# Performance work log

Hardware: AMD Instinct MI355X
Metric: run time of the kernel (lower is better)

The kernel has to match this reference:

```python
import jax, jax.numpy as jnp
import numpy as np

NUM_NODES = 10000  # fixed by input spec: edge_index values in [0, 10000)


def setup_inputs() -> dict:
    key = jax.random.key(0)
    k1, k2, k3 = jax.random.split(key, 3)
    N, E, D_IN, D_OUT = NUM_NODES, 320000, 256, 256
    x = jax.random.normal(k1, (N, D_IN), dtype=jnp.float32)
    edge_index = jax.random.randint(k2, (2, E), 0, N, dtype=jnp.int64)
    # ensure node N-1 appears so num_nodes == N as in the torch code
    edge_index = edge_index.at[0, 0].set(N - 1)
    # xavier_uniform for [D_IN, D_OUT]
    limit = float(np.sqrt(6.0 / (D_IN + D_OUT)))
    weight = jax.random.uniform(k3, (D_IN, D_OUT), dtype=jnp.float32,
                                minval=-limit, maxval=limit)
    return {"x": x, "edge_index": edge_index, "weight": weight}


def _normalize_adjacency(edge_index, num_nodes):
    src, dst = edge_index[0], edge_index[1]
    ones = jnp.ones(src.shape[0], dtype=jnp.float32)
    # symmetric binarized adjacency: adj[i,j] = adj[j,i] = 1 (set, not add)
    adj = jnp.zeros((num_nodes, num_nodes), dtype=jnp.float32)
    adj = adj.at[src, dst].max(ones)
    adj = adj.at[dst, src].max(ones)
    # one round of self-loops: adj += I
    adj = adj + jnp.eye(num_nodes, dtype=jnp.float32)
    deg = jnp.sum(adj, axis=1)                    # [N]
    dinv = 1.0 / jnp.sqrt(deg)                    # [N]
    # D^-1/2 A D^-1/2 via broadcasting (equivalent to diag mms)
    return adj * dinv[:, None] * dinv[None, :]


def reference(x, edge_index, weight):
    adj = _normalize_adjacency(edge_index, NUM_NODES)  # [N, N]
    h = adj @ x                                        # [N, D_IN]
    return h @ weight                                  # [N, D_OUT]
```

## Files before the change

### kernel.cpp

```cpp
#include <hip/hip_runtime.h>
#include <hip/hip_bf16.h>
#include <stdint.h>

#define N_NODES   10000
#define D_FEAT    256
#define E_EDGES   320000
#define ROW_WORDS 313
#define ROW_STRIDE 320
#define LIST_CAP  1024

#define NB    250
#define RPB   40
#define B_CAP 8192

#define LDSTR 264

typedef __attribute__((ext_vector_type(4))) float float4v;
typedef _Float16 half8  __attribute__((ext_vector_type(8)));
typedef _Float16 half4v __attribute__((ext_vector_type(4)));

__device__ __forceinline__ uint16_t f2bf(float f) {
    union { float f; uint32_t u; } v; v.f = f;
    uint32_t r = v.u + 0x7fffu + ((v.u >> 16) & 1u);
    return (uint16_t)(r >> 16);
}
__device__ __forceinline__ float lo16(uint32_t u) {
    union { uint32_t u; float f; } v; v.u = u << 16; return v.f;
}
__device__ __forceinline__ float hi16(uint32_t u) {
    union { uint32_t u; float f; } v; v.u = u & 0xffff0000u; return v.f;
}


__global__ void __launch_bounds__(1024)
fill_buckets(const int* __restrict__ ei, uint32_t* __restrict__ bucketbuf,
             uint32_t* __restrict__ cursors) {
    __shared__ uint32_t hist[256];
    __shared__ uint32_t lofs[256];
    __shared__ uint32_t base_s[256];
    __shared__ uint32_t stage[2048];
    __shared__ uint16_t sbkt[2048];
    int t = threadIdx.x;
    if (t < 256) hist[t] = 0;
    __syncthreads();
    int e = blockIdx.x * 1024 + t;
    int b0 = -1, b1 = -1; uint32_t ent0 = 0, ent1 = 0, s0 = 0, s1 = 0;
    if (e < E_EDGES) {
        int s = ei[e], d = ei[E_EDGES + e];
        if ((uint32_t)s < N_NODES && (uint32_t)d < N_NODES) {
            b0 = s / RPB; ent0 = ((uint32_t)(s - b0 * RPB) << 14) | (uint32_t)d;
            b1 = d / RPB; ent1 = ((uint32_t)(d - b1 * RPB) << 14) | (uint32_t)s;
            s0 = atomicAdd(&hist[b0], 1u);
            s1 = atomicAdd(&hist[b1], 1u);
        }
    }
    __syncthreads();
    if (t < 256) lofs[t] = hist[t];
    __syncthreads();
    for (int d = 1; d < 256; d <<= 1) {
        uint32_t v = 0;
        if (t < 256 && t >= d) v = lofs[t - d];
        __syncthreads();
        if (t < 256) lofs[t] += v;
        __syncthreads();
    }
    if (t < 256) base_s[t] = hist[t] ? atomicAdd(&cursors[t], hist[t]) : 0u;
    if (b0 >= 0) {
        uint32_t p0 = lofs[b0] - hist[b0] + s0;
        stage[p0] = ent0; sbkt[p0] = (uint16_t)b0;
        uint32_t p1 = lofs[b1] - hist[b1] + s1;
        stage[p1] = ent1; sbkt[p1] = (uint16_t)b1;
    }
    __syncthreads();
    uint32_t total = lofs[255];
    for (uint32_t idx = t; idx < total; idx += 1024) {
        uint32_t b = sbkt[idx];
        uint32_t pos = base_s[b] + (idx - (lofs[b] - hist[b]));
        if (pos < B_CAP) bucketbuf[(size_t)b * B_CAP + pos] = stage[idx];
    }
}

__global__ void __launch_bounds__(1024)
bucket_to_csr(const uint32_t* __restrict__ bucketbuf,
              const uint32_t* __restrict__ cursors,
              uint32_t* __restrict__ gcursor,
              uint32_t* __restrict__ col, uint32_t* __restrict__ row_base,
              uint32_t* __restrict__ row_deg, float* __restrict__ dinv) {
    __shared__ uint32_t bm[RPB * ROW_WORDS];
    __shared__ uint32_t degs[RPB];
    __shared__ uint32_t rowoff[RPB];
    __shared__ uint32_t segbase;
    int b = blockIdx.x, t = threadIdx.x;
    for (int i = t; i < RPB * ROW_WORDS; i += 1024) bm[i] = 0;
    __syncthreads();
    uint32_t cnt = min(cursors[b], (uint32_t)B_CAP);
    const uint32_t* bb = bucketbuf + (size_t)b * B_CAP;
    for (uint32_t i = t; i < cnt; i += 1024) {
        uint32_t ent = bb[i];
        uint32_t lr = ent >> 14, d = ent & 0x3FFFu;
        atomicOr(&bm[lr * ROW_WORDS + (d >> 5)], 1u << (d & 31));
    }
    __syncthreads();
    int wv = t >> 6, lane = t & 63;
    for (int r = wv; r < RPB; r += 16) {
        int pop = 0;
        #pragma unroll
        for (int k = 0; k < 5; k++) {
            int w = lane + 64 * k;
            if (w < ROW_WORDS) pop += __popc(bm[r * ROW_WORDS + w]);
        }
        #pragma unroll
        for (int off = 32; off > 0; off >>= 1) pop += __shfl_xor(pop, off, 64);
        if (lane == 0) degs[r] = (uint32_t)pop;
    }
    __syncthreads();
    if (t == 0) {
        uint32_t run = 0;
        for (int r = 0; r < RPB; r++) {
            rowoff[r] = run;
            run += (degs[r] + 3u) & ~3u;
        }
        segbase = atomicAdd(gcursor, run);
    }
    __syncthreads();
    int row0 = b * RPB;
    for (int r = wv; r < RPB; r += 16) {
        int gi = row0 + r;
        uint32_t base = segbase + rowoff[r];
        if (lane == 0) {
            row_base[gi] = base;
            row_deg[gi]  = degs[r];
            dinv[gi]     = 1.0f / sqrtf((float)(degs[r] + 1u));
        }
        uint32_t wb[5]; int tot = 0;
        #pragma unroll
        for (int k = 0; k < 5; k++) {
            int w = lane + 64 * k;
            uint32_t v = (w < ROW_WORDS) ? bm[r * ROW_WORDS + w] : 0u;
            wb[k] = v; tot += __popc(v);
        }
        int incl = tot;
        #pragma unroll
        for (int off = 1; off < 64; off <<= 1) {
            int v = __shfl_up(incl, off, 64);
            if (lane >= off) incl += v;
        }
        uint32_t p = base + (uint32_t)(incl - tot);
        #pragma unroll
        for (int k = 0; k < 5; k++) {
            uint32_t bits = wb[k];
            uint32_t cbase = (uint32_t)(lane + 64 * k) << 5;
            while (bits) {
                col[p++] = cbase + (uint32_t)__builtin_ctz(bits);
                bits &= bits - 1;
            }
        }
    }
}

__global__ void __launch_bounds__(256)
scale_cast(const float* __restrict__ dinv, const float* __restrict__ x,
           uint16_t* __restrict__ xs) {
    int wv = threadIdx.x >> 6, lane = threadIdx.x & 63;
    int i = blockIdx.x * 4 + wv;
    float di = dinv[i];
    float4v v = *(const float4v*)(x + (size_t)i * D_FEAT + lane * 4);
    uint2 o;
    o.x = (uint32_t)f2bf(di * v[0]) | ((uint32_t)f2bf(di * v[1]) << 16);
    o.y = (uint32_t)f2bf(di * v[2]) | ((uint32_t)f2bf(di * v[3]) << 16);
    *(uint2*)(xs + (size_t)i * D_FEAT + lane * 4) = o;
}

__global__ void __launch_bounds__(256)
wcast(const float* __restrict__ w, _Float16* __restrict__ wt) {
    int k = blockIdx.x, n = threadIdx.x;
    wt[(size_t)n * D_FEAT + k] = (_Float16)w[(size_t)k * D_FEAT + n];
}

__global__ void __launch_bounds__(256)
spmm_gemm(const uint32_t* __restrict__ row_base, const uint32_t* __restrict__ row_deg,
          const float* __restrict__ dinv, const uint32_t* __restrict__ col,
          const uint16_t* __restrict__ xs, const _Float16* __restrict__ wt,
          float* __restrict__ out) {
    __shared__ __align__(16) _Float16 a_lds[16 * LDSTR];
    int t = threadIdx.x, wv = t >> 6, lane = t & 63;
    int r0 = blockIdx.x * 16;
    size_t ch = (size_t)lane * 4;

    for (int rr = wv; rr < 16; rr += 4) {
        int i = r0 + rr;
        uint32_t base = row_base[i], deg = row_deg[i];
        float di = dinv[i];
        float4v z = {0.f, 0.f, 0.f, 0.f};
        float4v acc0 = z, acc1 = z, acc2 = z, acc3 = z;
        uint32_t t4 = deg & ~3u;
        for (uint32_t k = 0; k < t4; k += 4) {
            uint4 jv = *(const uint4*)&col[base + k];
            uint2 g0 = *(const uint2*)(xs + (size_t)jv.x * D_FEAT + ch);
            uint2 g1 = *(const uint2*)(xs + (size_t)jv.y * D_FEAT + ch);
            uint2 g2 = *(const uint2*)(xs + (size_t)jv.z * D_FEAT + ch);
            uint2 g3 = *(const uint2*)(xs + (size_t)jv.w * D_FEAT + ch);
            acc0[0] += lo16(g0.x); acc0[1] += hi16(g0.x); acc0[2] += lo16(g0.y); acc0[3] += hi16(g0.y);
            acc1[0] += lo16(g1.x); acc1[1] += hi16(g1.x); acc1[2] += lo16(g1.y); acc1[3] += hi16(g1.y);
            acc2[0] += lo16(g2.x); acc2[1] += hi16(g2.x); acc2[2] += lo16(g2.y); acc2[3] += hi16(g2.y);
            acc3[0] += lo16(g3.x); acc3[1] += hi16(g3.x); acc3[2] += lo16(g3.y); acc3[3] += hi16(g3.y);
        }
        for (uint32_t k = t4; k < deg; k++) {
            uint32_t j = col[base + k];
            uint2 g = *(const uint2*)(xs + (size_t)j * D_FEAT + ch);
            acc0[0] += lo16(g.x); acc0[1] += hi16(g.x); acc0[2] += lo16(g.y); acc0[3] += hi16(g.y);
        }
        uint2 gs = *(const uint2*)(xs + (size_t)i * D_FEAT + ch);
        acc1[0] += lo16(gs.x); acc1[1] += hi16(gs.x); acc1[2] += lo16(gs.y); acc1[3] += hi16(gs.y);
        float4v acc = (acc0 + acc1) + (acc2 + acc3);
        half4v o = { (_Float16)(di * acc[0]), (_Float16)(di * acc[1]),
                     (_Float16)(di * acc[2]), (_Float16)(di * acc[3]) };
        *(half4v*)&a_lds[rr * LDSTR + lane * 4] = o;
    }
    __syncthreads();

    int quad = lane >> 4, r = lane & 15;
    int mbase = r0 + quad * 4;
    #pragma unroll
    for (int u = 0; u < 4; u++) {
        int ct = wv * 4 + u;
        const _Float16* pb = wt + (size_t)(ct * 16 + r) * D_FEAT + quad * 8;
        float4v acc = {0.f, 0.f, 0.f, 0.f};
        #pragma unroll
        for (int kk = 0; kk < D_FEAT; kk += 32) {
            half8 a = *(const half8*)&a_lds[r * LDSTR + kk + quad * 8];
            half8 b = *(const half8*)(pb + kk);
            acc = __builtin_amdgcn_mfma_f32_16x16x32_f16(a, b, acc, 0, 0, 0);
        }
        int colg = ct * 16 + r;
        #pragma unroll
        for (int v = 0; v < 4; v++)
            out[(size_t)(mbase + v) * D_FEAT + colg] = acc[v];
    }
}


__global__ void scatter_edges_fb(const int* __restrict__ ei,
                                 uint32_t* __restrict__ bitmap) {
    int e = blockIdx.x * blockDim.x + threadIdx.x;
    if (e >= E_EDGES) return;
    int s = ei[e], d = ei[E_EDGES + e];
    if ((uint32_t)s >= N_NODES || (uint32_t)d >= N_NODES) return;
    atomicOr(&bitmap[(size_t)s * ROW_STRIDE + (d >> 5)], 1u << (d & 31));
    atomicOr(&bitmap[(size_t)d * ROW_STRIDE + (s >> 5)], 1u << (s & 31));
}

__global__ void __launch_bounds__(256)
popc_dinv(const uint32_t* __restrict__ bitmap, float* __restrict__ dinv) {
    int wv = threadIdx.x >> 6, lane = threadIdx.x & 63;
    int i = blockIdx.x * 4 + wv;
    const uint32_t* rb = bitmap + (size_t)i * ROW_STRIDE;
    int pop = 0;
    #pragma unroll
    for (int k = 0; k < 5; k++) {
        int w = lane + 64 * k;
        if (w < ROW_WORDS) pop += __popc(rb[w]);
    }
    #pragma unroll
    for (int off = 32; off > 0; off >>= 1) pop += __shfl_xor(pop, off, 64);
    if (lane == 0) dinv[i] = 1.0f / sqrtf((float)(pop + 1));
}

__global__ void __launch_bounds__(256)
spmm_bitmap_fb(const uint32_t* __restrict__ bitmap, const float* __restrict__ dinv,
               const float* __restrict__ xf, float* __restrict__ agg) {
    __shared__ __align__(16) uint32_t lists[4][LIST_CAP];
    int wv = threadIdx.x >> 6, lane = threadIdx.x & 63;
    int i = blockIdx.x * 4 + wv;
    uint32_t* list = lists[wv];
    const uint32_t* rb = bitmap + (size_t)i * ROW_STRIDE;

    uint32_t wbits[5]; int tot = 0;
    #pragma unroll
    for (int k = 0; k < 5; k++) {
        int w = lane + 64 * k;
        uint32_t b = (w < ROW_WORDS) ? rb[w] : 0u;
        wbits[k] = b;
        tot += __popc(b);
    }
    int incl = tot;
    #pragma unroll
    for (int off = 1; off < 64; off <<= 1) {
        int v = __shfl_up(incl, off, 64);
        if (lane >= off) incl += v;
    }
    uint32_t p = (uint32_t)(incl - tot);
    uint32_t deg = (uint32_t)__shfl(incl, 63, 64);
    #pragma unroll
    for (int k = 0; k < 5; k++) {
        uint32_t bits = wbits[k];
        uint32_t base = (uint32_t)(lane + 64 * k) << 5;
        while (bits) {
            if (p < LIST_CAP) list[p] = base + (uint32_t)__builtin_ctz(bits);
            p++;
            bits &= bits - 1;
        }
    }
    if (deg > LIST_CAP) deg = LIST_CAP;

    float di = dinv[i];
    float4v z = {0.f, 0.f, 0.f, 0.f};
    float4v acc0 = z, acc1 = z, acc2 = z, acc3 = z;
    float4v sv = *(const float4v*)(xf + (size_t)i * D_FEAT + lane * 4);
    uint32_t t4 = deg & ~3u;
    for (uint32_t k = 0; k < t4; k += 4) {
        uint4 jv = *(const uint4*)&list[k];
        float d0 = dinv[jv.x], d1 = dinv[jv.y], d2 = dinv[jv.z], d3 = dinv[jv.w];
        float4v v0 = *(const float4v*)(xf + (size_t)jv.x * D_FEAT + lane * 4);
        float4v v1 = *(const float4v*)(xf + (size_t)jv.y * D_FEAT + lane * 4);
        float4v v2 = *(const float4v*)(xf + (size_t)jv.z * D_FEAT + lane * 4);
        float4v v3 = *(const float4v*)(xf + (size_t)jv.w * D_FEAT + lane * 4);
        acc0 += d0 * v0; acc1 += d1 * v1; acc2 += d2 * v2; acc3 += d3 * v3;
    }
    for (uint32_t k = t4; k < deg; k++) {
        uint32_t j = list[k];
        acc0 += dinv[j] * (*(const float4v*)(xf + (size_t)j * D_FEAT + lane * 4));
    }
    float4v acc = (acc0 + acc1) + (acc2 + acc3) + di * sv;
    *(float4v*)(agg + (size_t)i * D_FEAT + lane * 4) = di * acc;
}

__global__ void __launch_bounds__(256)
gemm_valu(float* __restrict__ io, const float* __restrict__ wf) {
    __shared__ __align__(16) float a_lds[16 * D_FEAT];
    int c = threadIdx.x;
    int r0 = blockIdx.x * 16;
    for (int idx = c; idx < 16 * D_FEAT; idx += 256)
        a_lds[idx] = io[(size_t)r0 * D_FEAT + idx];
    __syncthreads();
    float acc[16];
    #pragma unroll
    for (int r = 0; r < 16; r++) acc[r] = 0.f;
    for (int k0 = 0; k0 < D_FEAT; k0 += 4) {
        float w0 = wf[(size_t)(k0 + 0) * D_FEAT + c];
        float w1 = wf[(size_t)(k0 + 1) * D_FEAT + c];
        float w2 = wf[(size_t)(k0 + 2) * D_FEAT + c];
        float w3 = wf[(size_t)(k0 + 3) * D_FEAT + c];
        #pragma unroll
        for (int r = 0; r < 16; r++) {
            float4v av = *(const float4v*)&a_lds[r * D_FEAT + k0];
            acc[r] = fmaf(av[3], w3, fmaf(av[2], w2,
                     fmaf(av[1], w1, fmaf(av[0], w0, acc[r]))));
        }
    }
    #pragma unroll
    for (int r = 0; r < 16; r++)
        io[(size_t)(r0 + r) * D_FEAT + c] = acc[r];
}

extern "C" void kernel_launch(void* const* d_in, const int* in_sizes, int n_in,
                              void* d_out, int out_size, void* d_ws, size_t ws_size,
                              hipStream_t stream) {
    const float* x  = (const float*)d_in[0];
    const int*   ei = (const int*)d_in[1];
    const float* w  = (const float*)d_in[2];
    float* out = (float*)d_out;
    uint8_t* ws = (uint8_t*)d_ws;

    const size_t CUR_OFF  = 8192000;
    const size_t RB_OFF   = 8194048;
    const size_t RD_OFF   = 8234048;
    const size_t DI_OFF   = 8274048;
    const size_t XS_OFF   = 8314048;
    const size_t COL_OFF  = 13434048;
    const size_t WT_OFF   = 16154048;
    const size_t NEED_NEW = 16285120;
    const size_t NEED_FB  = 12840000;

    if (ws_size >= NEED_NEW) {
        uint32_t* bucketbuf = (uint32_t*)ws;
        uint32_t* cursors   = (uint32_t*)(ws + CUR_OFF);
        uint32_t* row_base  = (uint32_t*)(ws + RB_OFF);
        uint32_t* row_deg   = (uint32_t*)(ws + RD_OFF);
        float*    dinv      = (float*)(ws + DI_OFF);
        uint16_t* xs        = (uint16_t*)(ws + XS_OFF);
        uint32_t* col       = (uint32_t*)(ws + COL_OFF);
        _Float16* wt        = (_Float16*)(ws + WT_OFF);

        hipMemsetAsync(cursors, 0, 2048, stream);
        fill_buckets <<<(E_EDGES + 1023) / 1024, 1024, 0, stream>>>(ei, bucketbuf, cursors);
        bucket_to_csr<<<NB, 1024, 0, stream>>>(bucketbuf, cursors, &cursors[NB],
                                               col, row_base, row_deg, dinv);
        wcast        <<<D_FEAT, D_FEAT, 0, stream>>>(w, wt);
        scale_cast   <<<N_NODES / 4, 256, 0, stream>>>(dinv, x, xs);
        spmm_gemm    <<<N_NODES / 16, 256, 0, stream>>>(row_base, row_deg, dinv,
                                                        col, xs, wt, out);
    } else if (ws_size >= NEED_FB) {
        uint32_t* bitmap = (uint32_t*)ws;
        float*    dinv   = (float*)(ws + 12800000);

        hipMemsetAsync(bitmap, 0, 12800000, stream);
        scatter_edges_fb<<<(E_EDGES + 255) / 256, 256, 0, stream>>>(ei, bitmap);
        popc_dinv      <<<N_NODES / 4, 256, 0, stream>>>(bitmap, dinv);
        spmm_bitmap_fb <<<N_NODES / 4, 256, 0, stream>>>(bitmap, dinv, x, out);
        gemm_valu      <<<N_NODES / 16, 256, 0, stream>>>(out, w);
    }
}
```

Before: 158.4 us.

## Fold weight cast and x scaling into CSR kernels, split SpMM from MFMA GEMM

The weight transpose and cast now run in extra blocks of fill_buckets, staged through LDS so the fp16 stores are vectorised. The dinv scaling and bf16 cast of x move into bucket_to_csr. The fused spmm_gemm kernel is split into a one-row-per-wave SpMM that writes fp16 aggregates into the reused bucket buffer, followed by a separate MFMA GEMM on a 2D grid. This removes two launches and gives the gather more parallelism, at the cost of an extra global round trip for the aggregated features.

New measurement: 142.7 us. 10.0% less time.

```diff
diff --git a/kernel.cpp b/kernel.cpp
--- a/kernel.cpp
+++ b/kernel.cpp
@@ -9,11 +9,11 @@
 #define ROW_STRIDE 320
 #define LIST_CAP  1024
 
-#define NB    250
-#define RPB   40
-#define B_CAP 8192
-
-#define LDSTR 264
+#define NB     250
+#define RPB    40
+#define B_CAP  8192
+#define NBLK_E 313
+#define NBLK_W 64
 
 typedef __attribute__((ext_vector_type(4))) float float4v;
 typedef _Float16 half8  __attribute__((ext_vector_type(8)));
@@ -34,13 +34,29 @@
 
 __global__ void __launch_bounds__(1024)
 fill_buckets(const int* __restrict__ ei, uint32_t* __restrict__ bucketbuf,
-             uint32_t* __restrict__ cursors) {
+             uint32_t* __restrict__ cursors,
+             const float* __restrict__ w, _Float16* __restrict__ wt) {
     __shared__ uint32_t hist[256];
     __shared__ uint32_t lofs[256];
     __shared__ uint32_t base_s[256];
     __shared__ uint32_t stage[2048];
     __shared__ uint16_t sbkt[2048];
     int t = threadIdx.x;
+
+    if (blockIdx.x >= NBLK_E) {
+        int kb = (blockIdx.x - NBLK_E) * 4;
+        int k = kb + (t >> 8), n = t & 255;
+        float* st = (float*)stage;
+        st[(n << 2) | (t >> 8)] = w[(size_t)k * D_FEAT + n];
+        __syncthreads();
+        if (t < 256) {
+            half4v o = { (_Float16)st[t * 4 + 0], (_Float16)st[t * 4 + 1],
+                         (_Float16)st[t * 4 + 2], (_Float16)st[t * 4 + 3] };
+            *(half4v*)&wt[(size_t)t * D_FEAT + kb] = o;
+        }
+        return;
+    }
+
     if (t < 256) hist[t] = 0;
     __syncthreads();
     int e = blockIdx.x * 1024 + t;
@@ -85,7 +101,8 @@
               const uint32_t* __restrict__ cursors,
               uint32_t* __restrict__ gcursor,
               uint32_t* __restrict__ col, uint32_t* __restrict__ row_base,
-              uint32_t* __restrict__ row_deg, float* __restrict__ dinv) {
+              uint32_t* __restrict__ row_deg, float* __restrict__ dinv,
+              const float* __restrict__ x, uint16_t* __restrict__ xs) {
     __shared__ uint32_t bm[RPB * ROW_WORDS];
     __shared__ uint32_t degs[RPB];
     __shared__ uint32_t rowoff[RPB];
@@ -127,11 +144,17 @@
     for (int r = wv; r < RPB; r += 16) {
         int gi = row0 + r;
         uint32_t base = segbase + rowoff[r];
+        float di = 1.0f / sqrtf((float)(degs[r] + 1u));
         if (lane == 0) {
             row_base[gi] = base;
             row_deg[gi]  = degs[r];
-            dinv[gi]     = 1.0f / sqrtf((float)(degs[r] + 1u));
-        }
+            dinv[gi]     = di;
+        }
+        float4v xv = *(const float4v*)(x + (size_t)gi * D_FEAT + lane * 4);
+        uint2 o;
+        o.x = (uint32_t)f2bf(di * xv[0]) | ((uint32_t)f2bf(di * xv[1]) << 16);
+        o.y = (uint32_t)f2bf(di * xv[2]) | ((uint32_t)f2bf(di * xv[3]) << 16);
+        *(uint2*)(xs + (size_t)gi * D_FEAT + lane * 4) = o;
         uint32_t wb[5]; int tot = 0;
         #pragma unroll
         for (int k = 0; k < 5; k++) {
@@ -159,84 +182,65 @@
 }
 
 __global__ void __launch_bounds__(256)
-scale_cast(const float* __restrict__ dinv, const float* __restrict__ x,
-           uint16_t* __restrict__ xs) {
+spmm_csr(const uint32_t* __restrict__ row_base, const uint32_t* __restrict__ row_deg,
+         const float* __restrict__ dinv, const uint32_t* __restrict__ col,
+         const uint16_t* __restrict__ xs, _Float16* __restrict__ aggh) {
     int wv = threadIdx.x >> 6, lane = threadIdx.x & 63;
     int i = blockIdx.x * 4 + wv;
+    uint32_t base = row_base[i], deg = row_deg[i];
     float di = dinv[i];
-    float4v v = *(const float4v*)(x + (size_t)i * D_FEAT + lane * 4);
-    uint2 o;
-    o.x = (uint32_t)f2bf(di * v[0]) | ((uint32_t)f2bf(di * v[1]) << 16);
-    o.y = (uint32_t)f2bf(di * v[2]) | ((uint32_t)f2bf(di * v[3]) << 16);
-    *(uint2*)(xs + (size_t)i * D_FEAT + lane * 4) = o;
+    float4v z = {0.f, 0.f, 0.f, 0.f};
+    float4v acc0 = z, acc1 = z, acc2 = z, acc3 = z;
+    size_t ch = (size_t)lane * 4;
+    uint32_t t4 = deg & ~3u;
+    for (uint32_t t = 0; t < t4; t += 4) {
+        uint4 jv = *(const uint4*)&col[base + t];
+        uint2 g0 = *(const uint2*)(xs + (size_t)jv.x * D_FEAT + ch);
+        uint2 g1 = *(const uint2*)(xs + (size_t)jv.y * D_FEAT + ch);
+        uint2 g2 = *(const uint2*)(xs + (size_t)jv.z * D_FEAT + ch);
+        uint2 g3 = *(const uint2*)(xs + (size_t)jv.w * D_FEAT + ch);
+        acc0[0] += lo16(g0.x); acc0[1] += hi16(g0.x); acc0[2] += lo16(g0.y); acc0[3] += hi16(g0.y);
+        acc1[0] += lo16(g1.x); acc1[1] += hi16(g1.x); acc1[2] += lo16(g1.y); acc1[3] += hi16(g1.y);
+        acc2[0] += lo16(g2.x); acc2[1] += hi16(g2.x); acc2[2] += lo16(g2.y); acc2[3] += hi16(g2.y);
+        acc3[0] += lo16(g3.x); acc3[1] += hi16(g3.x); acc3[2] += lo16(g3.y); acc3[3] += hi16(g3.y);
+    }
+    for (uint32_t t = t4; t < deg; t++) {
+        uint32_t j = col[base + t];
+        uint2 g = *(const uint2*)(xs + (size_t)j * D_FEAT + ch);
+        acc0[0] += lo16(g.x); acc0[1] += hi16(g.x); acc0[2] += lo16(g.y); acc0[3] += hi16(g.y);
+    }
+    uint2 gs = *(const uint2*)(xs + (size_t)i * D_FEAT + ch);
+    acc1[0] += lo16(gs.x); acc1[1] += hi16(gs.x); acc1[2] += lo16(gs.y); acc1[3] += hi16(gs.y);
+    float4v acc = (acc0 + acc1) + (acc2 + acc3);
+    half4v o = { (_Float16)(di * acc[0]), (_Float16)(di * acc[1]),
+                 (_Float16)(di * acc[2]), (_Float16)(di * acc[3]) };
+    *(half4v*)(aggh + (size_t)i * D_FEAT + ch) = o;
 }
 
 __global__ void __launch_bounds__(256)
-wcast(const float* __restrict__ w, _Float16* __restrict__ wt) {
-    int k = blockIdx.x, n = threadIdx.x;
-    wt[(size_t)n * D_FEAT + k] = (_Float16)w[(size_t)k * D_FEAT + n];
-}
-
-__global__ void __launch_bounds__(256)
-spmm_gemm(const uint32_t* __restrict__ row_base, const uint32_t* __restrict__ row_deg,
-          const float* __restrict__ dinv, const uint32_t* __restrict__ col,
-          const uint16_t* __restrict__ xs, const _Float16* __restrict__ wt,
+gemm_mfma(const _Float16* __restrict__ aggh, const _Float16* __restrict__ wt,
           float* __restrict__ out) {
-    __shared__ __align__(16) _Float16 a_lds[16 * LDSTR];
-    int t = threadIdx.x, wv = t >> 6, lane = t & 63;
-    int r0 = blockIdx.x * 16;
-    size_t ch = (size_t)lane * 4;
-
-    for (int rr = wv; rr < 16; rr += 4) {
-        int i = r0 + rr;
-        uint32_t base = row_base[i], deg = row_deg[i];
-        float di = dinv[i];
-        float4v z = {0.f, 0.f, 0.f, 0.f};
-        float4v acc0 = z, acc1 = z, acc2 = z, acc3 = z;
-        uint32_t t4 = deg & ~3u;
-        for (uint32_t k = 0; k < t4; k += 4) {
-            uint4 jv = *(const uint4*)&col[base + k];
-            uint2 g0 = *(const uint2*)(xs + (size_t)jv.x * D_FEAT + ch);
-            uint2 g1 = *(const uint2*)(xs + (size_t)jv.y * D_FEAT + ch);
-            uint2 g2 = *(const uint2*)(xs + (size_t)jv.z * D_FEAT + ch);
-            uint2 g3 = *(const uint2*)(xs + (size_t)jv.w * D_FEAT + ch);
-            acc0[0] += lo16(g0.x); acc0[1] += hi16(g0.x); acc0[2] += lo16(g0.y); acc0[3] += hi16(g0.y);
-            acc1[0] += lo16(g1.x); acc1[1] += hi16(g1.x); acc1[2] += lo16(g1.y); acc1[3] += hi16(g1.y);
-            acc2[0] += lo16(g2.x); acc2[1] += hi16(g2.x); acc2[2] += lo16(g2.y); acc2[3] += hi16(g2.y);
-            acc3[0] += lo16(g3.x); acc3[1] += hi16(g3.x); acc3[2] += lo16(g3.y); acc3[3] += hi16(g3.y);
-        }
-        for (uint32_t k = t4; k < deg; k++) {
-            uint32_t j = col[base + k];
-            uint2 g = *(const uint2*)(xs + (size_t)j * D_FEAT + ch);
-            acc0[0] += lo16(g.x); acc0[1] += hi16(g.x); acc0[2] += lo16(g.y); acc0[3] += hi16(g.y);
-        }
-        uint2 gs = *(const uint2*)(xs + (size_t)i * D_FEAT + ch);
-        acc1[0] += lo16(gs.x); acc1[1] += hi16(gs.x); acc1[2] += lo16(gs.y); acc1[3] += hi16(gs.y);
-        float4v acc = (acc0 + acc1) + (acc2 + acc3);
-        half4v o = { (_Float16)(di * acc[0]), (_Float16)(di * acc[1]),
-                     (_Float16)(di * acc[2]), (_Float16)(di * acc[3]) };
-        *(half4v*)&a_lds[rr * LDSTR + lane * 4] = o;
-    }
-    __syncthreads();
-
+    int t = threadIdx.x;
+    int wv = t >> 6, lane = t & 63;
     int quad = lane >> 4, r = lane & 15;
-    int mbase = r0 + quad * 4;
-    #pragma unroll
-    for (int u = 0; u < 4; u++) {
-        int ct = wv * 4 + u;
-        const _Float16* pb = wt + (size_t)(ct * 16 + r) * D_FEAT + quad * 8;
-        float4v acc = {0.f, 0.f, 0.f, 0.f};
-        #pragma unroll
-        for (int kk = 0; kk < D_FEAT; kk += 32) {
-            half8 a = *(const half8*)&a_lds[r * LDSTR + kk + quad * 8];
-            half8 b = *(const half8*)(pb + kk);
-            acc = __builtin_amdgcn_mfma_f32_16x16x32_f16(a, b, acc, 0, 0, 0);
-        }
-        int colg = ct * 16 + r;
-        #pragma unroll
-        for (int v = 0; v < 4; v++)
-            out[(size_t)(mbase + v) * D_FEAT + colg] = acc[v];
-    }
+    int bx = blockIdx.x;
+    int ct = blockIdx.y * 4 + wv;
+
+    const _Float16* pa = aggh + (size_t)(bx * 16 + r) * D_FEAT + quad * 8;
+    const _Float16* pb = wt   + (size_t)(ct * 16 + r) * D_FEAT + quad * 8;
+
+    float4v acc = {0.f, 0.f, 0.f, 0.f};
+    #pragma unroll
+    for (int kk = 0; kk < D_FEAT; kk += 32) {
+        half8 a = *(const half8*)(pa + kk);
+        half8 b = *(const half8*)(pb + kk);
+        acc = __builtin_amdgcn_mfma_f32_16x16x32_f16(a, b, acc, 0, 0, 0);
+    }
+    int mbase = bx * 16 + quad * 4;
+    int colg  = ct * 16 + r;
+    #pragma unroll
+    for (int u = 0; u < 4; u++)
+        out[(size_t)(mbase + u) * D_FEAT + colg] = acc[u];
 }
 
 
@@ -374,6 +378,7 @@
 
     if (ws_size >= NEED_NEW) {
         uint32_t* bucketbuf = (uint32_t*)ws;
+        _Float16* aggh      = (_Float16*)ws;
         uint32_t* cursors   = (uint32_t*)(ws + CUR_OFF);
         uint32_t* row_base  = (uint32_t*)(ws + RB_OFF);
         uint32_t* row_deg   = (uint32_t*)(ws + RD_OFF);
@@ -383,13 +388,11 @@
         _Float16* wt        = (_Float16*)(ws + WT_OFF);
 
         hipMemsetAsync(cursors, 0, 2048, stream);
-        fill_buckets <<<(E_EDGES + 1023) / 1024, 1024, 0, stream>>>(ei, bucketbuf, cursors);
+        fill_buckets <<<NBLK_E + NBLK_W, 1024, 0, stream>>>(ei, bucketbuf, cursors, w, wt);
         bucket_to_csr<<<NB, 1024, 0, stream>>>(bucketbuf, cursors, &cursors[NB],
-                                               col, row_base, row_deg, dinv);
-        wcast        <<<D_FEAT, D_FEAT, 0, stream>>>(w, wt);
-        scale_cast   <<<N_NODES / 4, 256, 0, stream>>>(dinv, x, xs);
-        spmm_gemm    <<<N_NODES / 16, 256, 0, stream>>>(row_base, row_deg, dinv,
-                                                        col, xs, wt, out);
+                                               col, row_base, row_deg, dinv, x, xs);
+        spmm_csr     <<<N_NODES / 4, 256, 0, stream>>>(row_base, row_deg, dinv, col, xs, aggh);
+        gemm_mfma    <<<dim3(N_NODES / 16, 4), 256, 0, stream>>>(aggh, wt, out);
     } else if (ws_size >= NEED_FB) {
         uint32_t* bitmap = (uint32_t*)ws;
         float*    dinv   = (float*)(ws + 12800000);
```
